# Optimization experiments

Measured on AMD Instinct MI355X. Metric: run time of the kernel, lower is better.

Reference implementation:

```python
import jax, jax.numpy as jnp
import numpy as np

EPS = 1e-5
SLOPE = 0.2  # LeakyReLU slope in ConvBlock


def _conv3d(x, W, b):
    # x: [N, Ci, D, H, W], W: [Co, Ci, 3, 3, 3], padding 1 (same)
    y = jax.lax.conv_general_dilated(
        x, W, window_strides=(1, 1, 1), padding=[(1, 1), (1, 1), (1, 1)],
        dimension_numbers=("NCDHW", "OIDHW", "NCDHW"))
    return y + b[None, :, None, None, None]


def _inorm(x):
    # InstanceNorm3d(affine=False): normalize over spatial dims per (N, C)
    m = jnp.mean(x, axis=(2, 3, 4), keepdims=True)
    v = jnp.var(x, axis=(2, 3, 4), keepdims=True)
    return (x - m) * jax.lax.rsqrt(v + EPS)


def _block(x, W, b):
    # Conv3d -> InstanceNorm3d -> LeakyReLU(0.2)
    return jax.nn.leaky_relu(_inorm(_conv3d(x, W, b)), SLOPE)


def _lin(x, W, b):
    # 1x1x1 conv == channel-mixing linear; x: [..., Ci, D, H, W], W: [Co, Ci]
    return jnp.einsum("oi,...idhw->...odhw", W, x) + b[:, None, None, None]


def setup_inputs() -> dict:
    key = jax.random.key(0)
    ks = jax.random.split(key, 12)
    B, T, Ci, Co, D = 1, 8, 1, 16, 64
    s_in = 1.0 / np.sqrt(Ci * 27)
    s_att = 1.0 / np.sqrt(Co)
    s_f = 1.0 / np.sqrt(Co * 27)
    return {
        "c": jax.random.normal(ks[0], (B, T, Ci, D, D, D), jnp.float32),
        "e": jax.random.normal(ks[1], (B, T, Ci, D, D, D), jnp.float32),
        "pos_emb": jax.random.normal(ks[2], (1, D, D, D), jnp.float32) * 0.02,
        "Wq": jax.random.normal(ks[3], (Co, Ci, 3, 3, 3), jnp.float32) * s_in,
        "bq": jnp.zeros((Co,), jnp.float32),
        "Wk": jax.random.normal(ks[4], (Co, Ci, 3, 3, 3), jnp.float32) * s_in,
        "bk": jnp.zeros((Co,), jnp.float32),
        "Wv": jax.random.normal(ks[5], (Co, Ci, 3, 3, 3), jnp.float32) * s_in,
        "bv": jnp.zeros((Co,), jnp.float32),
        "Wa1": jax.random.normal(ks[6], (Co, Co), jnp.float32) * s_att,
        "ba1": jnp.zeros((Co,), jnp.float32),
        "Wa2": jax.random.normal(ks[7], (Co, Co), jnp.float32) * s_att,
        "ba2": jnp.zeros((Co,), jnp.float32),
        "Wa3": jax.random.normal(ks[8], (Co, Co), jnp.float32) * s_att,
        "ba3": jnp.zeros((Co,), jnp.float32),
        "Wf": jax.random.normal(ks[9], (Co, Co, 3, 3, 3), jnp.float32) * s_f,
        "bf": jnp.zeros((Co,), jnp.float32),
    }


def reference(c, e, pos_emb, Wq, bq, Wk, bk, Wv, bv,
              Wa1, ba1, Wa2, ba2, Wa3, ba3, Wf, bf):
    B, T = c.shape[0], c.shape[1]
    c = c + pos_emb  # broadcast [1,D,H,W] over [B,T,Ci,D,H,W]
    e = e + pos_emb

    cf = c.reshape((B * T,) + c.shape[2:])
    ef = e.reshape((B * T,) + e.shape[2:])
    # per-frame q/k/v conv blocks, batched over all T frames at once
    def per_t(x):
        return jnp.moveaxis(x.reshape((B, T) + x.shape[1:]), 1, 0)  # [T,B,Co,D,H,W]

    q = per_t(_block(ef, Wq, bq))
    k = per_t(_block(cf, Wk, bk))
    v = per_t(_block(cf, Wv, bv))

    A = _lin(q, Wa1, ba1)   # conv1(q_i) for all i: [T,B,Co,D,H,W]
    Bk = _lin(k, Wa2, ba2)  # conv2(k_j) for all j

    def step(carry, xs):
        qi, Ai = xs  # [B,Co,D,H,W]
        # gating over all key frames at once: [T,B,Co,D,H,W]
        scale = jax.nn.sigmoid(_lin(jax.nn.relu(Ai + Bk), Wa3, ba3))
        out = jnp.sum(scale * v, axis=0)          # weighted sum over keys
        out = _block(out + qi, Wf, bf)            # conv_forward
        return carry, out

    _, outs = jax.lax.scan(step, None, (q, A))    # [T,B,Co,D,H,W]
    return jnp.swapaxes(outs, 0, 1)               # [B,T,Co,D,H,W]
```

## Files before the change

### kernel.cpp

```cpp
#include <hip/hip_runtime.h>
#include <hip/hip_bf16.h>
#include <math.h>


#define V18 (1 << 18)
#define SOFF (3 * (1 << 25))

typedef __attribute__((ext_vector_type(4))) _Float16 f16x4;
typedef __attribute__((ext_vector_type(8))) _Float16 f16x8;
typedef __attribute__((ext_vector_type(4))) float f32x4;

__device__ __forceinline__ float lrelu(float x) { return x > 0.f ? x : 0.2f * x; }
__device__ __forceinline__ float sigm(float x) {
  return __builtin_amdgcn_rcpf(1.f + __expf(-x));
}

__device__ __forceinline__ f32x4 mfma16(f16x4 a, f16x4 b, f32x4 c) {
  return __builtin_amdgcn_mfma_f32_16x16x16f16(a, b, c, 0, 0, 0);
}

__device__ __forceinline__ f16x4 frag_from_words(const uint* sp, int a) {
  uint2 t;
  t.x = sp[a];
  t.y = sp[a + 2];
  return __builtin_bit_cast(f16x4, t);
}

__device__ __forceinline__ void gload_lds16(const void* g, void* l) {
  __builtin_amdgcn_global_load_lds(
      (const __attribute__((address_space(1))) void*)g,
      (__attribute__((address_space(3))) void*)l, 16, 0, 0);
}

__global__ void k_prep(const float* __restrict__ Wq, const float* __restrict__ Wk,
                       const float* __restrict__ Wv, const float* __restrict__ Wf,
                       float* __restrict__ P) {
  int tid = threadIdx.x;
  _Float16* wf16 = (_Float16*)P;
  for (int i = tid; i < 7168; i += 256) {
    int h = i / 3584, r = i % 3584, p = r / 256, q_ = r & 255;
    int lane = q_ >> 2, j = q_ & 3;
    int co = lane & 15, kq = lane >> 4;
    int kk = kq * 4 + j, tp = kk >> 3, ci = h * 8 + (kk & 7), tap = p * 2 + tp;
    wf16[i] = (tap < 27) ? (_Float16)Wf[co * 432 + ci * 27 + tap] : (_Float16)0.f;
  }
  _Float16* wqkv = wf16 + 7168;
  for (int i = tid; i < 2304; i += 256) {
    int conv = i / 768, rem = i % 768, m = rem / 256, li = rem & 255;
    int lane = li >> 2, j = li & 3;
    int co = lane & 15, q_ = lane >> 4;
    int r = m * 4 + q_;
    const float* W = conv == 0 ? Wq : conv == 1 ? Wk : Wv;
    float val = 0.f;
    if (r <= 8 && j < 3) val = W[co * 27 + (r / 3) * 9 + (r % 3) * 3 + j];
    wqkv[i] = (_Float16)val;
  }
}

__global__ __launch_bounds__(256) void k1_qkv(
    const float* __restrict__ c, const float* __restrict__ e,
    const float* __restrict__ pos, const _Float16* __restrict__ wqkv,
    const float* __restrict__ bq, const float* __restrict__ bk,
    const float* __restrict__ bv, _Float16* __restrict__ q,
    _Float16* __restrict__ k, _Float16* __restrict__ v,
    float* __restrict__ gstats) {
  __shared__ __align__(16) uint seP[2592];
  __shared__ __align__(16) uint scP[2592];
  __shared__ float red[96];
  const int t = blockIdx.y;
  const int tile = blockIdx.x;
  const int y0 = (tile & 15) * 4;
  const int z0 = (tile >> 4) * 4;
  const int tid = threadIdx.x;
  const int lane = tid & 63, zw = tid >> 6;
  const int col = lane & 15, cq = lane >> 4;

  if (tid < 96) red[tid] = 0.f;

  _Float16* se16 = (_Float16*)seP;
  _Float16* sc16 = (_Float16*)scP;
  const float* cin = c + t * V18;
  const float* ein = e + t * V18;
  for (int i = tid; i < 2448; i += 256) {
    int rw = i / 68, lx = i % 68;
    int gz = z0 + rw / 6 - 1, gy = y0 + rw % 6 - 1, gx = lx - 1;
    float pe = 0.f, pc = 0.f;
    if (lx < 66 && (unsigned)gz < 64u && (unsigned)gy < 64u && (unsigned)gx < 64u) {
      int gi = (gz << 12) + (gy << 6) + gx;
      float pv = pos[gi];
      pc = cin[gi] + pv;
      pe = ein[gi] + pv;
    }
    const _Float16 he = (_Float16)pe, hc = (_Float16)pc;
    const int wp = rw * 72 + lx;
    se16[2 * wp] = he;
    sc16[2 * wp] = hc;
    if (i) {
      se16[2 * wp - 1] = he;
      sc16[2 * wp - 1] = hc;
    }
  }

  f16x4 wq_[3], wk_[3], wv_[3];
#pragma unroll
  for (int m = 0; m < 3; ++m) {
    wq_[m] = *(const f16x4*)&wqkv[(0 * 3 + m) * 256 + lane * 4];
    wk_[m] = *(const f16x4*)&wqkv[(1 * 3 + m) * 256 + lane * 4];
    wv_[m] = *(const f16x4*)&wqkv[(2 * 3 + m) * 256 + lane * 4];
  }
  const f32x4 bqv = *(const f32x4*)&bq[cq * 4];
  const f32x4 bkv = *(const f32x4*)&bk[cq * 4];
  const f32x4 bvv = *(const f32x4*)&bv[cq * 4];
  int rowoff[3];
#pragma unroll
  for (int m = 0; m < 3; ++m) {
    int r = m * 4 + cq;
    if (r > 8) r = 8;
    rowoff[m] = ((r / 3) * 6 + (r % 3)) * 72;
  }

  f32x4 sq = {0,0,0,0}, sq2 = {0,0,0,0}, sk = {0,0,0,0},
        sk2 = {0,0,0,0}, sv = {0,0,0,0}, sv2 = {0,0,0,0};

  __syncthreads();

#pragma unroll 8
  for (int g = 0; g < 16; ++g) {
    const int gy = g >> 2, xg = g & 3;
    const int base = (zw * 6 + gy) * 72 + xg * 16 + col;
    const int a0 = base + rowoff[0], a1 = base + rowoff[1], a2 = base + rowoff[2];
    f16x4 be0 = frag_from_words(seP, a0);
    f16x4 be1 = frag_from_words(seP, a1);
    f16x4 be2 = frag_from_words(seP, a2);
    f16x4 bc0 = frag_from_words(scP, a0);
    f16x4 bc1 = frag_from_words(scP, a1);
    f16x4 bc2 = frag_from_words(scP, a2);

    f32x4 qa = mfma16(wq_[0], be0, bqv);
    qa = mfma16(wq_[1], be1, qa);
    qa = mfma16(wq_[2], be2, qa);
    f32x4 ka = mfma16(wk_[0], bc0, bkv);
    ka = mfma16(wk_[1], bc1, ka);
    ka = mfma16(wk_[2], bc2, ka);
    f32x4 va = mfma16(wv_[0], bc0, bvv);
    va = mfma16(wv_[1], bc1, va);
    va = mfma16(wv_[2], bc2, va);

    const size_t vox = ((size_t)(z0 + zw) << 12) + ((y0 + gy) << 6) + xg * 16 + col;
    const size_t poff = ((size_t)(t * 4 + cq) << 20) + vox * 4;
    *(f16x4*)&q[poff] = (f16x4){(_Float16)qa[0], (_Float16)qa[1],
                                (_Float16)qa[2], (_Float16)qa[3]};
    *(f16x4*)&k[poff] = (f16x4){(_Float16)ka[0], (_Float16)ka[1],
                                (_Float16)ka[2], (_Float16)ka[3]};
    *(f16x4*)&v[poff] = (f16x4){(_Float16)va[0], (_Float16)va[1],
                                (_Float16)va[2], (_Float16)va[3]};
    sq += qa; sq2 += qa * qa;
    sk += ka; sk2 += ka * ka;
    sv += va; sv2 += va * va;
  }

#pragma unroll
  for (int d = 1; d < 16; d <<= 1) {
#pragma unroll
    for (int j = 0; j < 4; ++j) {
      sq[j] += __shfl_xor(sq[j], d);  sq2[j] += __shfl_xor(sq2[j], d);
      sk[j] += __shfl_xor(sk[j], d);  sk2[j] += __shfl_xor(sk2[j], d);
      sv[j] += __shfl_xor(sv[j], d);  sv2[j] += __shfl_xor(sv2[j], d);
    }
  }
  if (col == 0) {
#pragma unroll
    for (int j = 0; j < 4; ++j) {
      const int co = cq * 4 + j;
      atomicAdd(&red[co * 2], sq[j]);
      atomicAdd(&red[co * 2 + 1], sq2[j]);
      atomicAdd(&red[32 + co * 2], sk[j]);
      atomicAdd(&red[32 + co * 2 + 1], sk2[j]);
      atomicAdd(&red[64 + co * 2], sv[j]);
      atomicAdd(&red[64 + co * 2 + 1], sv2[j]);
    }
  }
  __syncthreads();
  if (tid < 96) {
    const int conv = tid >> 5, rem = tid & 31;
    atomicAdd(&gstats[(conv * 128 + t * 16) * 2 + rem], red[tid]);
  }
}

__global__ void k_finstats(const float* __restrict__ sums, float* __restrict__ mr,
                           _Float16* __restrict__ ah, _Float16* __restrict__ bh,
                           int n, float invn) {
  int i = blockIdx.x * blockDim.x + threadIdx.x;
  if (i >= n) return;
  float m = sums[i * 2] * invn;
  float var = sums[i * 2 + 1] * invn - m * m;
  float rs = rsqrtf(fmaxf(var, 0.f) + 1e-5f);
  mr[i * 2] = m;
  mr[i * 2 + 1] = rs;
  if (ah) {
    ah[i] = (_Float16)rs;
    bh[i] = (_Float16)(-m * rs);
  }
}

__global__ __launch_bounds__(256) void k2_attn(
    const _Float16* __restrict__ q, const _Float16* __restrict__ k,
    const _Float16* __restrict__ v, const float* __restrict__ Wa1,
    const float* __restrict__ Wa2, const float* __restrict__ Wa3,
    const _Float16* __restrict__ ah, const _Float16* __restrict__ bh,
    const float* __restrict__ ba1, const float* __restrict__ ba2,
    const float* __restrict__ ba3, _Float16* __restrict__ u) {
  const int lane = threadIdx.x & 63;
  const int wid = threadIdx.x >> 6;
  const int row = lane & 15;
  const int cq = lane >> 4;
  const int c0 = cq * 4;
  const int vox = (blockIdx.x * 4 + wid) * 16 + row;
  const _Float16 h02 = (_Float16)0.2f;
  const f16x4 hz = {(_Float16)0.f, (_Float16)0.f, (_Float16)0.f, (_Float16)0.f};

  f32x4 w1f = *(const f32x4*)&Wa1[row * 16 + c0];
  f32x4 w2f = *(const f32x4*)&Wa2[row * 16 + c0];
  f32x4 w3f = *(const f32x4*)&Wa3[row * 16 + c0];
  f16x4 wa1 = {(_Float16)w1f[0], (_Float16)w1f[1], (_Float16)w1f[2], (_Float16)w1f[3]};
  f16x4 wa2 = {(_Float16)w2f[0], (_Float16)w2f[1], (_Float16)w2f[2], (_Float16)w2f[3]};
  f16x4 wa3 = {(_Float16)w3f[0], (_Float16)w3f[1], (_Float16)w3f[2], (_Float16)w3f[3]};
  f32x4 b1q = *(const f32x4*)&ba1[c0];
  f32x4 b2q = *(const f32x4*)&ba2[c0];
  f32x4 b3q = *(const f32x4*)&ba3[c0];

  f32x4 acc[8];
  f16x4 ahalf[8], qn[8];
#pragma unroll
  for (int t = 0; t < 8; ++t) {
    f16x4 qh = *(const f16x4*)&q[((size_t)(t * 4 + cq) << 20) + (size_t)vox * 4];
    f16x4 a4 = *(const f16x4*)&ah[t * 16 + c0];
    f16x4 b4 = *(const f16x4*)&bh[t * 16 + c0];
    f16x4 x = qh * a4 + b4;
    qn[t] = __builtin_elementwise_max(x, x * h02);
    f32x4 A = mfma16(wa1, qn[t], b1q);
    ahalf[t] = (f16x4){(_Float16)A[0], (_Float16)A[1], (_Float16)A[2], (_Float16)A[3]};
    acc[t] = (f32x4){0.f, 0.f, 0.f, 0.f};
  }
#pragma unroll 1
  for (int j = 0; j < 8; ++j) {
    f16x4 kh = *(const f16x4*)&k[((size_t)(j * 4 + cq) << 20) + (size_t)vox * 4];
    f16x4 vh = *(const f16x4*)&v[((size_t)(j * 4 + cq) << 20) + (size_t)vox * 4];
    f16x4 ka = *(const f16x4*)&ah[128 + j * 16 + c0];
    f16x4 kb = *(const f16x4*)&bh[128 + j * 16 + c0];
    f16x4 va = *(const f16x4*)&ah[256 + j * 16 + c0];
    f16x4 vb = *(const f16x4*)&bh[256 + j * 16 + c0];
    f16x4 xk = kh * ka + kb;
    f16x4 kn = __builtin_elementwise_max(xk, xk * h02);
    f16x4 xv = vh * va + vb;
    f16x4 vn = __builtin_elementwise_max(xv, xv * h02);
    f32x4 vnf = {(float)vn[0], (float)vn[1], (float)vn[2], (float)vn[3]};
    f32x4 B = mfma16(wa2, kn, b2q);
    f16x4 bhh = {(_Float16)B[0], (_Float16)B[1], (_Float16)B[2], (_Float16)B[3]};
#pragma unroll
    for (int i = 0; i < 8; ++i) {
      f16x4 rel = ahalf[i] + bhh;
      f16x4 rh = __builtin_elementwise_max(rel, hz);
      f32x4 s = mfma16(wa3, rh, b3q);
      acc[i][0] += sigm(s[0]) * vnf[0];
      acc[i][1] += sigm(s[1]) * vnf[1];
      acc[i][2] += sigm(s[2]) * vnf[2];
      acc[i][3] += sigm(s[3]) * vnf[3];
    }
  }
#pragma unroll
  for (int t = 0; t < 8; ++t) {
    f16x4 acch = {(_Float16)acc[t][0], (_Float16)acc[t][1],
                  (_Float16)acc[t][2], (_Float16)acc[t][3]};
    f16x4 uh = acch + qn[t];
    *(f16x4*)&u[((size_t)t << 22) + ((size_t)vox << 4) + c0] = uh;
  }
}

__global__ __launch_bounds__(256) void k3_conv(
    const _Float16* __restrict__ u16, const _Float16* __restrict__ wf16,
    const float* __restrict__ bfv, _Float16* __restrict__ y16,
    float* __restrict__ fsums, const float* __restrict__ zpad) {
  __shared__ __align__(16) _Float16 sx[2432 * 8];
  __shared__ float red[32];
  const int t = blockIdx.y;
  int tile = blockIdx.x;
  tile = (tile & 7) * 32 + (tile >> 3);
  const int y0 = (tile & 15) * 4;
  const int z0 = (tile >> 4) * 4;
  const int tid = threadIdx.x;
  const int lane = tid & 63, wv = tid >> 6, zw = wv;

  if (tid < 32) red[tid] = 0.f;

  const int colv = lane & 15;
  const int tp = lane >> 5;
  const int ciq = ((lane >> 4) & 1) * 4;

  f32x4 bq = *(const f32x4*)&bfv[(lane >> 4) * 4];
  f32x4 acc[16];
#pragma unroll
  for (int g = 0; g < 16; ++g) acc[g] = bq;

  const _Float16* ubase = u16 + ((size_t)t << 22);

#pragma unroll 1
  for (int h = 0; h < 2; ++h) {
    if (h) __syncthreads();

    f16x4 wfr[14];
#pragma unroll
    for (int p = 0; p < 14; ++p)
      wfr[p] = *(const f16x4*)&wf16[(h * 14 + p) * 256 + lane * 4];

#pragma unroll 1
    for (int it = 0; it < 9; ++it) {
      const int i = it * 256 + tid;
      const int rw = i / 66, xs = i % 66;
      const int gz = z0 + rw / 6 - 1, gy = y0 + rw % 6 - 1, gx = xs - 1;
      const bool ok = (unsigned)gz < 64u && (unsigned)gy < 64u && (unsigned)gx < 64u;
      const void* src = ok
          ? (const void*)&ubase[(((gz << 12) + (gy << 6) + gx) << 4) + h * 8]
          : (const void*)zpad;
      gload_lds16(src, (void*)&sx[(it * 256 + wv * 64) * 8]);
    }
    if (tid < 128) {
      const int i = 2304 + tid;
      const int rw = i / 66, xs = i % 66;
      const int gz = z0 + rw / 6 - 1, gy = y0 + rw % 6 - 1, gx = xs - 1;
      const bool ok = i < 2376 && (unsigned)gz < 64u && (unsigned)gy < 64u &&
                      (unsigned)gx < 64u;
      const void* src = ok
          ? (const void*)&ubase[(((gz << 12) + (gy << 6) + gx) << 4) + h * 8]
          : (const void*)zpad;
      gload_lds16(src, (void*)&sx[(2304 + (tid >> 6) * 64) * 8]);
    }
    __syncthreads();

#pragma unroll
    for (int p = 0; p < 14; ++p) {
      f16x4 w = wfr[p];
      int tap = p * 2 + tp;
      if (tap > 26) tap = 26;
      const int dz = tap / 9, dy = (tap % 9) / 3, dx = tap % 3;
      const int base_p = (((zw + dz) * 6 + dy) * 66 + colv + dx) * 8 + ciq;
#pragma unroll
      for (int g = 0; g < 16; ++g) {
        f16x4 b = *(const f16x4*)&sx[base_p + ((g >> 2) * 66 + (g & 3) * 16) * 8];
        acc[g] = mfma16(w, b, acc[g]);
      }
    }
  }

  float s[4] = {0.f, 0.f, 0.f, 0.f}, s2[4] = {0.f, 0.f, 0.f, 0.f};
  _Float16* ybase = y16 + ((size_t)t << 22);
#pragma unroll
  for (int g = 0; g < 16; ++g) {
    const int gvox = ((z0 + zw) << 12) + ((y0 + (g >> 2)) << 6) + (g & 3) * 16 + colv;
    f16x4 o = {(_Float16)acc[g][0], (_Float16)acc[g][1],
               (_Float16)acc[g][2], (_Float16)acc[g][3]};
    *(f16x4*)&ybase[(gvox << 4) + (lane >> 4) * 4] = o;
#pragma unroll
    for (int j = 0; j < 4; ++j) {
      s[j] += acc[g][j];
      s2[j] += acc[g][j] * acc[g][j];
    }
  }
#pragma unroll
  for (int d = 1; d < 16; d <<= 1)
#pragma unroll
    for (int j = 0; j < 4; ++j) {
      s[j] += __shfl_xor(s[j], d);
      s2[j] += __shfl_xor(s2[j], d);
    }
  if ((lane & 15) == 0) {
    const int co0 = (lane >> 4) * 4;
#pragma unroll
    for (int j = 0; j < 4; ++j) {
      atomicAdd(&red[(co0 + j) * 2], s[j]);
      atomicAdd(&red[(co0 + j) * 2 + 1], s2[j]);
    }
  }
  __syncthreads();
  if (tid < 32) atomicAdd(&fsums[t * 32 + tid], red[tid]);
}

__global__ __launch_bounds__(256) void k4_norm(const _Float16* __restrict__ y16,
                                               const float* __restrict__ fmr,
                                               float* __restrict__ out) {
  const int t = blockIdx.x >> 8;
  const int vb = (blockIdx.x & 255) << 10;
  const _Float16* yb = y16 + ((size_t)t << 22);
  float* ob = out + ((size_t)t << 22);
  const float* f = fmr + t * 32;
#pragma unroll 1
  for (int it = 0; it < 4; ++it) {
    const int voxl = vb + it * 256 + threadIdx.x;
    f16x8 h0 = *(const f16x8*)&yb[voxl << 4];
    f16x8 h1 = *(const f16x8*)&yb[(voxl << 4) + 8];
#pragma unroll
    for (int co = 0; co < 8; ++co)
      ob[(co << 18) + voxl] = lrelu(((float)h0[co] - f[co * 2]) * f[co * 2 + 1]);
#pragma unroll
    for (int co = 0; co < 8; ++co)
      ob[((co + 8) << 18) + voxl] =
          lrelu(((float)h1[co] - f[(co + 8) * 2]) * f[(co + 8) * 2 + 1]);
  }
}

extern "C" void kernel_launch(void* const* d_in, const int* in_sizes, int n_in,
                              void* d_out, int out_size, void* d_ws, size_t ws_size,
                              hipStream_t stream) {
  const float* c = (const float*)d_in[0];
  const float* e = (const float*)d_in[1];
  const float* pos = (const float*)d_in[2];
  const float* Wq = (const float*)d_in[3];
  const float* bq = (const float*)d_in[4];
  const float* Wk = (const float*)d_in[5];
  const float* bk = (const float*)d_in[6];
  const float* Wv = (const float*)d_in[7];
  const float* bv = (const float*)d_in[8];
  const float* Wa1 = (const float*)d_in[9];
  const float* ba1 = (const float*)d_in[10];
  const float* Wa2 = (const float*)d_in[11];
  const float* ba2 = (const float*)d_in[12];
  const float* Wa3 = (const float*)d_in[13];
  const float* ba3 = (const float*)d_in[14];
  const float* Wf = (const float*)d_in[15];
  const float* bf_ = (const float*)d_in[16];

  float* ws = (float*)d_ws;
  _Float16* q16 = (_Float16*)ws;
  _Float16* k16 = q16 + ((size_t)1 << 25);
  _Float16* v16 = q16 + ((size_t)2 << 25);
  _Float16* y16 = (_Float16*)ws;
  float* stats = ws + SOFF;
  float* fsums = stats + 768;
  float* zpad = stats + 1024;
  float* qkvmr = stats + 1040;
  float* fmr = stats + 1808;
  _Float16* ah = (_Float16*)(stats + 2064);
  _Float16* bh = (_Float16*)(stats + 2256);
  float* P = stats + 2448;
  _Float16* wf16 = (_Float16*)P;
  _Float16* wqkv = wf16 + 7168;
  _Float16* u16 = (_Float16*)d_out;

  hipMemsetAsync(stats, 0, 1040 * sizeof(float), stream);
  hipLaunchKernelGGL(k_prep, dim3(1), dim3(256), 0, stream, Wq, Wk, Wv, Wf, P);
  hipLaunchKernelGGL(k1_qkv, dim3(256, 8), dim3(256), 0, stream,
                     c, e, pos, wqkv, bq, bk, bv, q16, k16, v16, stats);
  hipLaunchKernelGGL(k_finstats, dim3(2), dim3(256), 0, stream,
                     stats, qkvmr, ah, bh, 384, 1.f / 262144.f);
  hipLaunchKernelGGL(k2_attn, dim3(4096), dim3(256), 0, stream,
                     q16, k16, v16, Wa1, Wa2, Wa3, ah, bh, ba1, ba2, ba3, u16);
  hipLaunchKernelGGL(k3_conv, dim3(256, 8), dim3(256), 0, stream,
                     u16, wf16, bf_, y16, fsums, zpad);
  hipLaunchKernelGGL(k_finstats, dim3(1), dim3(256), 0, stream,
                     fsums, fmr, (_Float16*)nullptr, (_Float16*)nullptr,
                     128, 1.f / 262144.f);
  hipLaunchKernelGGL(k4_norm, dim3(2048), dim3(256), 0, stream, y16, fmr,
                     (float*)d_out);
}
```

Baseline: 277.3 us.

## Load both channel halves into LDS at once in conv; use exp2 sigmoid

In the final conv kernel, both 8-channel halves of the haloed input tile go into a doubled LDS buffer in a single pass, and all 28 weight fragments are loaded up front. This removes the second load phase and the barrier between halves, letting more loads be in flight. In exchange LDS use doubles, which the launch bounds of 2 blocks per CU are meant to accommodate, and register pressure rises. The attention kernel folds -log2(e) into Wa3 and ba3 so the sigmoid uses a raw exp2 instead of expf.

```diff
diff --git a/kernel.cpp b/kernel.cpp
--- a/kernel.cpp
+++ b/kernel.cpp
@@ -11,9 +11,6 @@
 typedef __attribute__((ext_vector_type(4))) float f32x4;
 
 __device__ __forceinline__ float lrelu(float x) { return x > 0.f ? x : 0.2f * x; }
-__device__ __forceinline__ float sigm(float x) {
-  return __builtin_amdgcn_rcpf(1.f + __expf(-x));
-}
 
 __device__ __forceinline__ f32x4 mfma16(f16x4 a, f16x4 b, f32x4 c) {
   return __builtin_amdgcn_mfma_f32_16x16x16f16(a, b, c, 0, 0, 0);
@@ -218,16 +215,19 @@
   const int vox = (blockIdx.x * 4 + wid) * 16 + row;
   const _Float16 h02 = (_Float16)0.2f;
   const f16x4 hz = {(_Float16)0.f, (_Float16)0.f, (_Float16)0.f, (_Float16)0.f};
+  const float nl2e = -1.44269504f;
 
   f32x4 w1f = *(const f32x4*)&Wa1[row * 16 + c0];
   f32x4 w2f = *(const f32x4*)&Wa2[row * 16 + c0];
   f32x4 w3f = *(const f32x4*)&Wa3[row * 16 + c0];
   f16x4 wa1 = {(_Float16)w1f[0], (_Float16)w1f[1], (_Float16)w1f[2], (_Float16)w1f[3]};
   f16x4 wa2 = {(_Float16)w2f[0], (_Float16)w2f[1], (_Float16)w2f[2], (_Float16)w2f[3]};
-  f16x4 wa3 = {(_Float16)w3f[0], (_Float16)w3f[1], (_Float16)w3f[2], (_Float16)w3f[3]};
+  f16x4 wa3 = {(_Float16)(w3f[0] * nl2e), (_Float16)(w3f[1] * nl2e),
+               (_Float16)(w3f[2] * nl2e), (_Float16)(w3f[3] * nl2e)};
   f32x4 b1q = *(const f32x4*)&ba1[c0];
   f32x4 b2q = *(const f32x4*)&ba2[c0];
-  f32x4 b3q = *(const f32x4*)&ba3[c0];
+  f32x4 b3f = *(const f32x4*)&ba3[c0];
+  f32x4 b3q = {b3f[0] * nl2e, b3f[1] * nl2e, b3f[2] * nl2e, b3f[3] * nl2e};
 
   f32x4 acc[8];
   f16x4 ahalf[8], qn[8];
@@ -262,10 +262,11 @@
       f16x4 rel = ahalf[i] + bhh;
       f16x4 rh = __builtin_elementwise_max(rel, hz);
       f32x4 s = mfma16(wa3, rh, b3q);
-      acc[i][0] += sigm(s[0]) * vnf[0];
-      acc[i][1] += sigm(s[1]) * vnf[1];
-      acc[i][2] += sigm(s[2]) * vnf[2];
-      acc[i][3] += sigm(s[3]) * vnf[3];
+#pragma unroll
+      for (int ch = 0; ch < 4; ++ch) {
+        float sg = __builtin_amdgcn_rcpf(1.f + __builtin_amdgcn_exp2f(s[ch]));
+        acc[i][ch] += sg * vnf[ch];
+      }
     }
   }
 #pragma unroll
@@ -277,11 +278,11 @@
   }
 }
 
-__global__ __launch_bounds__(256) void k3_conv(
+__global__ __launch_bounds__(256, 2) void k3_conv(
     const _Float16* __restrict__ u16, const _Float16* __restrict__ wf16,
     const float* __restrict__ bfv, _Float16* __restrict__ y16,
     float* __restrict__ fsums, const float* __restrict__ zpad) {
-  __shared__ __align__(16) _Float16 sx[2432 * 8];
+  __shared__ __align__(16) _Float16 sx[4864 * 8];
   __shared__ float red[32];
   const int t = blockIdx.y;
   int tile = blockIdx.x;
@@ -297,53 +298,44 @@
   const int tp = lane >> 5;
   const int ciq = ((lane >> 4) & 1) * 4;
 
+  const _Float16* ubase = u16 + ((size_t)t << 22);
+
+#pragma unroll 1
+  for (int it = 0; it < 19; ++it) {
+    const int i = it * 256 + wv * 64 + lane;
+    const int h = i >= 2432 ? 1 : 0;
+    const int s = i - h * 2432;
+    const int rw = s / 66, xs = s % 66;
+    const int gz = z0 + rw / 6 - 1, gy = y0 + rw % 6 - 1, gx = xs - 1;
+    const bool ok = s < 2376 && (unsigned)gz < 64u && (unsigned)gy < 64u &&
+                    (unsigned)gx < 64u;
+    const void* src = ok
+        ? (const void*)&ubase[(((gz << 12) + (gy << 6) + gx) << 4) + h * 8]
+        : (const void*)zpad;
+    gload_lds16(src, (void*)&sx[(it * 256 + wv * 64) * 8]);
+  }
+
+  f16x4 wfr[28];
+#pragma unroll
+  for (int p = 0; p < 28; ++p)
+    wfr[p] = *(const f16x4*)&wf16[p * 256 + lane * 4];
   f32x4 bq = *(const f32x4*)&bfv[(lane >> 4) * 4];
   f32x4 acc[16];
 #pragma unroll
   for (int g = 0; g < 16; ++g) acc[g] = bq;
 
-  const _Float16* ubase = u16 + ((size_t)t << 22);
+  __syncthreads();
 
 #pragma unroll 1
   for (int h = 0; h < 2; ++h) {
-    if (h) __syncthreads();
-
-    f16x4 wfr[14];
-#pragma unroll
-    for (int p = 0; p < 14; ++p)
-      wfr[p] = *(const f16x4*)&wf16[(h * 14 + p) * 256 + lane * 4];
-
-#pragma unroll 1
-    for (int it = 0; it < 9; ++it) {
-      const int i = it * 256 + tid;
-      const int rw = i / 66, xs = i % 66;
-      const int gz = z0 + rw / 6 - 1, gy = y0 + rw % 6 - 1, gx = xs - 1;
-      const bool ok = (unsigned)gz < 64u && (unsigned)gy < 64u && (unsigned)gx < 64u;
-      const void* src = ok
-          ? (const void*)&ubase[(((gz << 12) + (gy << 6) + gx) << 4) + h * 8]
-          : (const void*)zpad;
-      gload_lds16(src, (void*)&sx[(it * 256 + wv * 64) * 8]);
-    }
-    if (tid < 128) {
-      const int i = 2304 + tid;
-      const int rw = i / 66, xs = i % 66;
-      const int gz = z0 + rw / 6 - 1, gy = y0 + rw % 6 - 1, gx = xs - 1;
-      const bool ok = i < 2376 && (unsigned)gz < 64u && (unsigned)gy < 64u &&
-                      (unsigned)gx < 64u;
-      const void* src = ok
-          ? (const void*)&ubase[(((gz << 12) + (gy << 6) + gx) << 4) + h * 8]
-          : (const void*)zpad;
-      gload_lds16(src, (void*)&sx[(2304 + (tid >> 6) * 64) * 8]);
-    }
-    __syncthreads();
-
 #pragma unroll
     for (int p = 0; p < 14; ++p) {
-      f16x4 w = wfr[p];
+      f16x4 w = wfr[h * 14 + p];
       int tap = p * 2 + tp;
       if (tap > 26) tap = 26;
       const int dz = tap / 9, dy = (tap % 9) / 3, dx = tap % 3;
-      const int base_p = (((zw + dz) * 6 + dy) * 66 + colv + dx) * 8 + ciq;
+      const int base_p =
+          h * 19456 + (((zw + dz) * 6 + dy) * 66 + colv + dx) * 8 + ciq;
 #pragma unroll
       for (int g = 0; g < 16; ++g) {
         f16x4 b = *(const f16x4*)&sx[base_p + ((g >> 2) * 66 + (g & 3) * 16) * 8];
```

After: 301.7 us. 1.09x slower.

## Use 16x16x32 MFMA for forward conv and fold log2e into sigmoid weights

Applied to the files above, without the earlier changes.

The forward 3x3x3 conv switches from the 16x16x16 f16 MFMA to the 16x16x32 variant. Each instruction now covers 4 taps x 8 channels, which halves the MFMA count and uses 8-wide LDS reads with precomputed tap offsets. The weight prep kernel is rewritten for the new fragment layout. In the attention kernel, the gating weights and bias are prescaled by -log2(e), so the sigmoid uses exp2 directly and a multiply per element is dropped. Risks include the new layout matching and a larger weight buffer that shifts the wqkv offset.

```diff
diff --git a/kernel.cpp b/kernel.cpp
--- a/kernel.cpp
+++ b/kernel.cpp
@@ -11,12 +11,12 @@
 typedef __attribute__((ext_vector_type(4))) float f32x4;
 
 __device__ __forceinline__ float lrelu(float x) { return x > 0.f ? x : 0.2f * x; }
-__device__ __forceinline__ float sigm(float x) {
-  return __builtin_amdgcn_rcpf(1.f + __expf(-x));
-}
 
 __device__ __forceinline__ f32x4 mfma16(f16x4 a, f16x4 b, f32x4 c) {
   return __builtin_amdgcn_mfma_f32_16x16x16f16(a, b, c, 0, 0, 0);
+}
+__device__ __forceinline__ f32x4 mfma32(f16x8 a, f16x8 b, f32x4 c) {
+  return __builtin_amdgcn_mfma_f32_16x16x32_f16(a, b, c, 0, 0, 0);
 }
 
 __device__ __forceinline__ f16x4 frag_from_words(const uint* sp, int a) {
@@ -37,14 +37,13 @@
                        float* __restrict__ P) {
   int tid = threadIdx.x;
   _Float16* wf16 = (_Float16*)P;
-  for (int i = tid; i < 7168; i += 256) {
-    int h = i / 3584, r = i % 3584, p = r / 256, q_ = r & 255;
-    int lane = q_ >> 2, j = q_ & 3;
-    int co = lane & 15, kq = lane >> 4;
-    int kk = kq * 4 + j, tp = kk >> 3, ci = h * 8 + (kk & 7), tap = p * 2 + tp;
+  for (int i = tid; i < 28672; i += 256) {
+    int j = i & 7, lane = (i >> 3) & 255, tg = (i >> 11) % 7, h = i / 14336;
+    int co = lane & 15, q_ = lane >> 4;
+    int tap = tg * 4 + q_, ci = h * 8 + j;
     wf16[i] = (tap < 27) ? (_Float16)Wf[co * 432 + ci * 27 + tap] : (_Float16)0.f;
   }
-  _Float16* wqkv = wf16 + 7168;
+  _Float16* wqkv = wf16 + 28672;
   for (int i = tid; i < 2304; i += 256) {
     int conv = i / 768, rem = i % 768, m = rem / 256, li = rem & 255;
     int lane = li >> 2, j = li & 3;
@@ -218,16 +217,19 @@
   const int vox = (blockIdx.x * 4 + wid) * 16 + row;
   const _Float16 h02 = (_Float16)0.2f;
   const f16x4 hz = {(_Float16)0.f, (_Float16)0.f, (_Float16)0.f, (_Float16)0.f};
+  const float nl2e = -1.44269504f;
 
   f32x4 w1f = *(const f32x4*)&Wa1[row * 16 + c0];
   f32x4 w2f = *(const f32x4*)&Wa2[row * 16 + c0];
   f32x4 w3f = *(const f32x4*)&Wa3[row * 16 + c0];
   f16x4 wa1 = {(_Float16)w1f[0], (_Float16)w1f[1], (_Float16)w1f[2], (_Float16)w1f[3]};
   f16x4 wa2 = {(_Float16)w2f[0], (_Float16)w2f[1], (_Float16)w2f[2], (_Float16)w2f[3]};
-  f16x4 wa3 = {(_Float16)w3f[0], (_Float16)w3f[1], (_Float16)w3f[2], (_Float16)w3f[3]};
+  f16x4 wa3 = {(_Float16)(w3f[0] * nl2e), (_Float16)(w3f[1] * nl2e),
+               (_Float16)(w3f[2] * nl2e), (_Float16)(w3f[3] * nl2e)};
   f32x4 b1q = *(const f32x4*)&ba1[c0];
   f32x4 b2q = *(const f32x4*)&ba2[c0];
-  f32x4 b3q = *(const f32x4*)&ba3[c0];
+  f32x4 b3f = *(const f32x4*)&ba3[c0];
+  f32x4 b3q = {b3f[0] * nl2e, b3f[1] * nl2e, b3f[2] * nl2e, b3f[3] * nl2e};
 
   f32x4 acc[8];
   f16x4 ahalf[8], qn[8];
@@ -262,10 +264,11 @@
       f16x4 rel = ahalf[i] + bhh;
       f16x4 rh = __builtin_elementwise_max(rel, hz);
       f32x4 s = mfma16(wa3, rh, b3q);
-      acc[i][0] += sigm(s[0]) * vnf[0];
-      acc[i][1] += sigm(s[1]) * vnf[1];
-      acc[i][2] += sigm(s[2]) * vnf[2];
-      acc[i][3] += sigm(s[3]) * vnf[3];
+#pragma unroll
+      for (int ch = 0; ch < 4; ++ch) {
+        float sg = __builtin_amdgcn_rcpf(1.f + __builtin_amdgcn_exp2f(s[ch]));
+        acc[i][ch] += sg * vnf[ch];
+      }
     }
   }
 #pragma unroll
@@ -294,10 +297,18 @@
   if (tid < 32) red[tid] = 0.f;
 
   const int colv = lane & 15;
-  const int tp = lane >> 5;
-  const int ciq = ((lane >> 4) & 1) * 4;
-
-  f32x4 bq = *(const f32x4*)&bfv[(lane >> 4) * 4];
+  const int tq = lane >> 4;
+
+  int offt[7];
+#pragma unroll
+  for (int tg = 0; tg < 7; ++tg) {
+    int tap = tg * 4 + tq;
+    if (tap > 26) tap = 26;
+    const int dz = tap / 9, dy = (tap % 9) / 3, dx = tap % 3;
+    offt[tg] = ((zw + dz) * 6 + dy) * 66 + dx;
+  }
+
+  f32x4 bq = *(const f32x4*)&bfv[tq * 4];
   f32x4 acc[16];
 #pragma unroll
   for (int g = 0; g < 16; ++g) acc[g] = bq;
@@ -308,10 +319,10 @@
   for (int h = 0; h < 2; ++h) {
     if (h) __syncthreads();
 
-    f16x4 wfr[14];
-#pragma unroll
-    for (int p = 0; p < 14; ++p)
-      wfr[p] = *(const f16x4*)&wf16[(h * 14 + p) * 256 + lane * 4];
+    f16x8 wfr[7];
+#pragma unroll
+    for (int tg = 0; tg < 7; ++tg)
+      wfr[tg] = *(const f16x8*)&wf16[((h * 7 + tg) * 256 + lane) * 8];
 
 #pragma unroll 1
     for (int it = 0; it < 9; ++it) {
@@ -338,16 +349,14 @@
     __syncthreads();
 
 #pragma unroll
-    for (int p = 0; p < 14; ++p) {
-      f16x4 w = wfr[p];
-      int tap = p * 2 + tp;
-      if (tap > 26) tap = 26;
-      const int dz = tap / 9, dy = (tap % 9) / 3, dx = tap % 3;
-      const int base_p = (((zw + dz) * 6 + dy) * 66 + colv + dx) * 8 + ciq;
+    for (int tg = 0; tg < 7; ++tg) {
+      const f16x8 w = wfr[tg];
+      const int bofft = offt[tg];
 #pragma unroll
       for (int g = 0; g < 16; ++g) {
-        f16x4 b = *(const f16x4*)&sx[base_p + ((g >> 2) * 66 + (g & 3) * 16) * 8];
-        acc[g] = mfma16(w, b, acc[g]);
+        f16x8 b = *(const f16x8*)
+            &sx[(bofft + (g >> 2) * 66 + (g & 3) * 16 + colv) * 8];
+        acc[g] = mfma32(w, b, acc[g]);
       }
     }
   }
@@ -359,7 +368,7 @@
     const int gvox = ((z0 + zw) << 12) + ((y0 + (g >> 2)) << 6) + (g & 3) * 16 + colv;
     f16x4 o = {(_Float16)acc[g][0], (_Float16)acc[g][1],
                (_Float16)acc[g][2], (_Float16)acc[g][3]};
-    *(f16x4*)&ybase[(gvox << 4) + (lane >> 4) * 4] = o;
+    *(f16x4*)&ybase[(gvox << 4) + tq * 4] = o;
 #pragma unroll
     for (int j = 0; j < 4; ++j) {
       s[j] += acc[g][j];
@@ -374,7 +383,7 @@
       s2[j] += __shfl_xor(s2[j], d);
     }
   if ((lane & 15) == 0) {
-    const int co0 = (lane >> 4) * 4;
+    const int co0 = tq * 4;
 #pragma unroll
     for (int j = 0; j < 4; ++j) {
       atomicAdd(&red[(co0 + j) * 2], s[j]);
@@ -443,7 +452,7 @@
   _Float16* bh = (_Float16*)(stats + 2256);
   float* P = stats + 2448;
   _Float16* wf16 = (_Float16*)P;
-  _Float16* wqkv = wf16 + 7168;
+  _Float16* wqkv = wf16 + 28672;
   _Float16* u16 = (_Float16*)d_out;
 
   hipMemsetAsync(stats, 0, 1040 * sizeof(float), stream);
```

Result: faster. 263.2 us (median of 2 runs) (-5.1%).
